# Kernel tuning notes

Hardware: AMD Instinct MI355X
Metric: run time of the kernel (lower is better)

## Reference

```python
import jax, jax.numpy as jnp
import numpy as np

N = 50000      # nodes
E = 800000     # directed edges (before self-loops)
FEAT = 120     # raw node feature dim
TOPO = 8       # topological feature dim
H1, D1 = 8, 8  # conv1: heads, per-head dim
C = 40         # out_channels (classes)
NEG_SLOPE = 0.2


def setup_inputs() -> dict:
    key = jax.random.key(0)
    ks = jax.random.split(key, 10)
    return {
        "x": jax.random.normal(ks[0], (N, FEAT), dtype=jnp.float32),
        "topo": jax.random.normal(ks[1], (N, TOPO), dtype=jnp.float32),
        "edge_index": jax.random.randint(ks[2], (2, E), 0, N, dtype=jnp.int32),
        "W1": jax.random.normal(ks[3], (FEAT + TOPO, H1 * D1), dtype=jnp.float32) * 0.1,
        "a_src1": jax.random.normal(ks[4], (H1, D1), dtype=jnp.float32) * 0.1,
        "a_dst1": jax.random.normal(ks[5], (H1, D1), dtype=jnp.float32) * 0.1,
        "b1": jnp.zeros((H1 * D1,), dtype=jnp.float32),
        "W2": jax.random.normal(ks[6], (H1 * D1, C), dtype=jnp.float32) * 0.1,
        "a_src2": jax.random.normal(ks[7], (1, C), dtype=jnp.float32) * 0.1,
        "a_dst2": jax.random.normal(ks[8], (1, C), dtype=jnp.float32) * 0.1,
        "b2": jnp.zeros((C,), dtype=jnp.float32),
    }


def gat_conv(x, src, dst, W, a_src, a_dst, b, heads, d, concat):
    """PyG-style GATConv (eval mode). src/dst already include self-loops."""
    n = x.shape[0]
    h = (x @ W).reshape(n, heads, d)                      # [N,H,D]
    al_src = jnp.sum(h * a_src[None], axis=-1)            # [N,H]
    al_dst = jnp.sum(h * a_dst[None], axis=-1)            # [N,H]
    e = jax.nn.leaky_relu(al_src[src] + al_dst[dst], NEG_SLOPE)  # [E',H]
    # segment softmax over incoming edges per destination node
    m = jax.ops.segment_max(e, dst, num_segments=n)       # [N,H]
    p = jnp.exp(e - m[dst])                               # [E',H]
    s = jax.ops.segment_sum(p, dst, num_segments=n)       # [N,H]
    alpha = p / s[dst]                                    # [E',H]
    out = jax.ops.segment_sum(alpha[:, :, None] * h[src], dst, num_segments=n)  # [N,H,D]
    if concat:
        return out.reshape(n, heads * d) + b
    return out.mean(axis=1) + b


def reference(x, topo, edge_index, W1, a_src1, a_dst1, b1, W2, a_src2, a_dst2, b2):
    n = x.shape[0]
    loops = jnp.arange(n, dtype=edge_index.dtype)
    src = jnp.concatenate([edge_index[0], loops])
    dst = jnp.concatenate([edge_index[1], loops])
    xin = jnp.concatenate([x, topo], axis=1)              # [N, FEAT+TOPO]
    h = jax.nn.elu(gat_conv(xin, src, dst, W1, a_src1, a_dst1, b1, H1, D1, True))
    out = gat_conv(h, src, dst, W2, a_src2, a_dst2, b2, 1, C, False)
    return jax.nn.log_softmax(out, axis=1)
```

## Files before the change

### kernel.cpp

```cpp
#include <hip/hip_runtime.h>
#include <hip/hip_fp16.h>

#define NN 50000
#define EE 800000
#define NBUCK 196
#define CAP 5120
#define TILEA 1024
#define NBA ((EE + TILEA - 1) / TILEA)
#define NGB 782
#define SRCS_MAX (EE + 8 * NN)

typedef _Float16 half8 __attribute__((ext_vector_type(8)));
typedef float floatx4 __attribute__((ext_vector_type(4)));

__global__ void k_prep(const float* __restrict__ W1, const float* __restrict__ W2,
                       _Float16* __restrict__ Bf1, _Float16* __restrict__ Bf2,
                       int* __restrict__ cursor, float* __restrict__ alsrc,
                       float* __restrict__ al2s) {
    int tid = blockIdx.x * 256 + threadIdx.x;
    if (tid < 1024) {
        int kk = tid >> 8, ct = (tid >> 6) & 3, L = tid & 63;
        int k0 = kk * 32 + (L >> 4) * 8, col = ct * 16 + (L & 15);
        half8 v;
        #pragma unroll
        for (int j = 0; j < 8; j++) v[j] = (_Float16)W1[(k0 + j) * 64 + col];
        *(half8*)(Bf1 + ((size_t)((kk * 4 + ct) * 64 + L)) * 8) = v;
    } else if (tid < 1024 + 384) {
        int u = tid - 1024;
        int kk = u / 192, rem = u % 192;
        int ct = rem >> 6, L = rem & 63;
        int k0 = kk * 32 + (L >> 4) * 8, col = ct * 16 + (L & 15);
        half8 v;
        #pragma unroll
        for (int j = 0; j < 8; j++)
            v[j] = (col < 40) ? (_Float16)W2[(k0 + j) * 40 + col] : (_Float16)0.f;
        *(half8*)(Bf2 + ((size_t)((kk * 3 + ct) * 64 + L)) * 8) = v;
    } else {
        int u = tid - 1408;
        if (u < NBUCK) cursor[u] = 0;
        if (u >= 200 && u < 208) alsrc[(size_t)NN * 8 + (u - 200)] = -1e30f;
        if (u == 208) al2s[NN] = -1e30f;
    }
}

__global__ __launch_bounds__(256) void k_fusedAG(
    const int* __restrict__ ei, int* __restrict__ cursor,
    unsigned* __restrict__ bucketData,
    const float* __restrict__ x, const float* __restrict__ topo,
    const _Float16* __restrict__ Bf1,
    const float* __restrict__ a_src, const float* __restrict__ a_dst,
    __half* __restrict__ h1, float* __restrict__ alsrc, float* __restrict__ aldst) {
    if (blockIdx.x < NBA) {
        __shared__ int cnt[NBUCK], base[NBUCK];
        int t = threadIdx.x;
        for (int i = t; i < NBUCK; i += 256) cnt[i] = 0;
        __syncthreads();
        int e0 = blockIdx.x * TILEA;
        int nE = min(TILEA, EE - e0);
        unsigned pk[4]; int bk[4], rk[4];
        int m = 0;
        for (int i = t; i < nE; i += 256) {
            int e = e0 + i;
            int s = ei[e], d = ei[EE + e];
            pk[m] = ((unsigned)d << 16) | (unsigned)s;
            bk[m] = d >> 8;
            rk[m] = atomicAdd(&cnt[bk[m]], 1);
            m++;
        }
        __syncthreads();
        for (int i = t; i < NBUCK; i += 256)
            base[i] = (cnt[i] > 0) ? atomicAdd(&cursor[i], cnt[i]) : 0;
        __syncthreads();
        for (int k = 0; k < m; k++) {
            int pos = base[bk[k]] + rk[k];
            if (pos < CAP) bucketData[(size_t)bk[k] * CAP + pos] = pk[k];
        }
        return;
    }
    int wave = threadIdx.x >> 6, lane = threadIdx.x & 63;
    int row0 = (blockIdx.x - NBA) * 64 + wave * 16;
    if (row0 >= NN) return;
    int g = lane >> 4, li = lane & 15;
    int myrow = row0 + li;
    half8 B[16];
    const half8* bp = (const half8*)Bf1;
    #pragma unroll
    for (int i = 0; i < 16; i++) B[i] = bp[i * 64 + lane];
    floatx4 acc[4] = {{0,0,0,0},{0,0,0,0},{0,0,0,0},{0,0,0,0}};
    #pragma unroll
    for (int kk = 0; kk < 4; kk++) {
        int k0 = kk * 32 + g * 8;
        const float* sp = (k0 == 120) ? (topo + (size_t)myrow * 8)
                                      : (x + (size_t)myrow * 120 + k0);
        float4 u0 = ((const float4*)sp)[0];
        float4 u1 = ((const float4*)sp)[1];
        half8 av;
        av[0] = (_Float16)u0.x; av[1] = (_Float16)u0.y;
        av[2] = (_Float16)u0.z; av[3] = (_Float16)u0.w;
        av[4] = (_Float16)u1.x; av[5] = (_Float16)u1.y;
        av[6] = (_Float16)u1.z; av[7] = (_Float16)u1.w;
        #pragma unroll
        for (int ct = 0; ct < 4; ct++)
            acc[ct] = __builtin_amdgcn_mfma_f32_16x16x32_f16(av, B[kk * 4 + ct], acc[ct], 0, 0, 0);
    }
    #pragma unroll
    for (int ct = 0; ct < 4; ct++)
        #pragma unroll
        for (int r = 0; r < 4; r++)
            h1[(size_t)(row0 + 4 * g + r) * 64 + ct * 16 + li] = __float2half(acc[ct][r]);
    float ps[4][4], pd[4][4];
    #pragma unroll
    for (int ct = 0; ct < 4; ct++) {
        int head = 2 * ct + (li >> 3), dix = li & 7;
        float asv = a_src[head * 8 + dix];
        float adv = a_dst[head * 8 + dix];
        #pragma unroll
        for (int r = 0; r < 4; r++) {
            ps[ct][r] = acc[ct][r] * asv;
            pd[ct][r] = acc[ct][r] * adv;
        }
    }
    #pragma unroll
    for (int off = 1; off <= 4; off <<= 1)
        #pragma unroll
        for (int ct = 0; ct < 4; ct++)
            #pragma unroll
            for (int r = 0; r < 4; r++) {
                ps[ct][r] += __shfl_xor(ps[ct][r], off, 64);
                pd[ct][r] += __shfl_xor(pd[ct][r], off, 64);
            }
    if ((li & 7) == 0) {
        #pragma unroll
        for (int ct = 0; ct < 4; ct++) {
            int head = 2 * ct + (li >> 3);
            #pragma unroll
            for (int r = 0; r < 4; r++) {
                int row = row0 + 4 * g + r;
                alsrc[row * 8 + head] = ps[ct][r];
                aldst[row * 8 + head] = pd[ct][r];
            }
        }
    }
}

__global__ __launch_bounds__(1024) void k_bucketB(const unsigned* __restrict__ bucketData,
        const int* __restrict__ cursor,
        int2* __restrict__ rowseg, int* __restrict__ srcs) {
    __shared__ int cnt[256], cur[256], sbuf[256], svals[256];
    __shared__ int sorted[CAP + 2048];
    int b = blockIdx.x, t = threadIdx.x;
    int nloc = min(256, NN - b * 256);
    int ecnt = min(cursor[b], CAP);
    size_t inBase = (size_t)b * CAP;
    if (t < 256) {
        int vv = 0;
        if (t < NBUCK) {
            int nl = min(256, NN - t * 256);
            vv = min(cursor[t], CAP) + 8 * nl;
        }
        svals[t] = vv;
    }
    __syncthreads();
    int* a = svals; int* bb = sbuf;
    for (int off = 1; off < 256; off <<= 1) {
        if (t < 256) bb[t] = a[t] + ((t >= off) ? a[t - off] : 0);
        __syncthreads();
        int* tmp = a; a = bb; bb = tmp;
    }
    int outBase = (b == 0) ? 0 : a[b - 1];
    __syncthreads();
    if (t < 256) cnt[t] = (t < nloc) ? 1 : 0;
    __syncthreads();
    for (int i = t; i < ecnt; i += 1024) {
        unsigned u = bucketData[inBase + i];
        atomicAdd(&cnt[(u >> 16) & 255], 1);
    }
    __syncthreads();
    int cv = 0, pcv = 0;
    if (t < 256) {
        cv = cnt[t];
        pcv = (t < nloc) ? ((cv + 7) & ~7) : 0;
        sbuf[t] = pcv;
    }
    __syncthreads();
    a = sbuf; bb = cnt;
    for (int off = 1; off < 256; off <<= 1) {
        if (t < 256) bb[t] = a[t] + ((t >= off) ? a[t - off] : 0);
        __syncthreads();
        int* tmp = a; a = bb; bb = tmp;
    }
    int total = a[255];
    int excl = (t < 256) ? (a[t] - pcv) : 0;
    __syncthreads();
    if (t < nloc) {
        rowseg[b * 256 + t] = make_int2(outBase + excl, outBase + excl + pcv);
        sorted[excl] = b * 256 + t;
        for (int k = cv; k < pcv; k++) sorted[excl + k] = NN;
        cur[t] = excl + 1;
    }
    __syncthreads();
    for (int i = t; i < ecnt; i += 1024) {
        unsigned u = bucketData[inBase + i];
        int ld = (u >> 16) & 255;
        int p = atomicAdd(&cur[ld], 1);
        sorted[p] = (int)(u & 0xffffu);
    }
    __syncthreads();
    for (int i = t; i < total; i += 1024) srcs[outBase + i] = sorted[i];
}

__global__ __launch_bounds__(256) void k_agg1(
    const int2* __restrict__ rowseg, const int* __restrict__ srcs,
    const float* __restrict__ alsrc, const float* __restrict__ aldst,
    const __half* __restrict__ h1, const float* __restrict__ b1,
    __half* __restrict__ hout) {
    int wave = threadIdx.x >> 6;
    int lane = threadIdx.x & 63;
    int d = blockIdx.x * 4 + wave;
    if (d >= NN) return;
    int hs = lane >> 5;
    int cp = lane & 31;
    int hh = cp >> 2;
    float adst = aldst[d * 8 + hh];
    int2 seg = rowseg[d];
    int jb = seg.x, je = seg.y;
    float ssum = 0.f, ax = 0.f, ay = 0.f;
    int sA0 = srcs[jb + hs],     sA1 = srcs[jb + 2 + hs];
    int sA2 = srcs[jb + 4 + hs], sA3 = srcs[jb + 6 + hs];
    for (int j = jb; j < je; j += 8) {
        int s0 = sA0, s1 = sA1, s2 = sA2, s3 = sA3;
        int jn = j + 8;
        if (jn < je) {
            sA0 = srcs[jn + hs];     sA1 = srcs[jn + 2 + hs];
            sA2 = srcs[jn + 4 + hs]; sA3 = srcs[jn + 6 + hs];
        }
        float e0 = alsrc[s0 * 8 + hh] + adst;
        float e1 = alsrc[s1 * 8 + hh] + adst;
        float e2 = alsrc[s2 * 8 + hh] + adst;
        float e3 = alsrc[s3 * 8 + hh] + adst;
        __half2 v0 = *(const __half2*)(h1 + (size_t)s0 * 64 + 2 * cp);
        __half2 v1 = *(const __half2*)(h1 + (size_t)s1 * 64 + 2 * cp);
        __half2 v2 = *(const __half2*)(h1 + (size_t)s2 * 64 + 2 * cp);
        __half2 v3 = *(const __half2*)(h1 + (size_t)s3 * 64 + 2 * cp);
        float p0 = __expf(fmaxf(e0, 0.2f * e0));
        float p1 = __expf(fmaxf(e1, 0.2f * e1));
        float p2 = __expf(fmaxf(e2, 0.2f * e2));
        float p3 = __expf(fmaxf(e3, 0.2f * e3));
        float2 f0 = __half22float2(v0), f1 = __half22float2(v1);
        float2 f2 = __half22float2(v2), f3 = __half22float2(v3);
        ssum += (p0 + p1) + (p2 + p3);
        ax += p0 * f0.x + p1 * f1.x + p2 * f2.x + p3 * f3.x;
        ay += p0 * f0.y + p1 * f1.y + p2 * f2.y + p3 * f3.y;
    }
    ssum += __shfl_xor(ssum, 32, 64);
    ax += __shfl_xor(ax, 32, 64);
    ay += __shfl_xor(ay, 32, 64);
    if (hs == 0) {
        float2 bv = *(const float2*)(b1 + 2 * cp);
        float inv = 1.f / ssum;
        float vx = ax * inv + bv.x;
        float vy = ay * inv + bv.y;
        vx = (vx > 0.f) ? vx : (__expf(vx) - 1.f);
        vy = (vy > 0.f) ? vy : (__expf(vy) - 1.f);
        *(__half2*)(hout + (size_t)d * 64 + 2 * cp) = __floats2half2_rn(vx, vy);
    }
}

__global__ __launch_bounds__(256) void k_gemm2(
    const __half* __restrict__ hout, const _Float16* __restrict__ Bf2,
    const float* __restrict__ a_src2, const float* __restrict__ a_dst2,
    __half* __restrict__ h2, float* __restrict__ al2s, float* __restrict__ al2d) {
    int wave = threadIdx.x >> 6, lane = threadIdx.x & 63;
    int row0 = blockIdx.x * 64 + wave * 16;
    if (row0 >= NN) return;
    int g = lane >> 4, li = lane & 15;
    int myrow = row0 + li;
    half8 B[6];
    const half8* bp = (const half8*)Bf2;
    #pragma unroll
    for (int i = 0; i < 6; i++) B[i] = bp[i * 64 + lane];
    floatx4 acc[3] = {{0,0,0,0},{0,0,0,0},{0,0,0,0}};
    #pragma unroll
    for (int kk = 0; kk < 2; kk++) {
        int k0 = kk * 32 + g * 8;
        half8 av = *(const half8*)(hout + (size_t)myrow * 64 + k0);
        #pragma unroll
        for (int ct = 0; ct < 3; ct++)
            acc[ct] = __builtin_amdgcn_mfma_f32_16x16x32_f16(av, B[kk * 3 + ct], acc[ct], 0, 0, 0);
    }
    float ts[4] = {0.f, 0.f, 0.f, 0.f}, td[4] = {0.f, 0.f, 0.f, 0.f};
    #pragma unroll
    for (int ct = 0; ct < 3; ct++) {
        int col = ct * 16 + li;
        bool ok = (col < 40);
        float asv = ok ? a_src2[col] : 0.f;
        float adv = ok ? a_dst2[col] : 0.f;
        #pragma unroll
        for (int r = 0; r < 4; r++) {
            ts[r] += acc[ct][r] * asv;
            td[r] += acc[ct][r] * adv;
            if (ok) h2[(size_t)(row0 + 4 * g + r) * 40 + col] = __float2half(acc[ct][r]);
        }
    }
    #pragma unroll
    for (int off = 1; off <= 8; off <<= 1)
        #pragma unroll
        for (int r = 0; r < 4; r++) {
            ts[r] += __shfl_xor(ts[r], off, 64);
            td[r] += __shfl_xor(td[r], off, 64);
        }
    if (li == 0) {
        #pragma unroll
        for (int r = 0; r < 4; r++) {
            int row = row0 + 4 * g + r;
            al2s[row] = ts[r];
            al2d[row] = td[r];
        }
    }
}

__global__ __launch_bounds__(256) void k_agg2(
    const int2* __restrict__ rowseg, const int* __restrict__ srcs,
    const float* __restrict__ al2s, const float* __restrict__ al2d,
    const __half* __restrict__ h2, const float* __restrict__ b2,
    float* __restrict__ out) {
    int wave = threadIdx.x >> 6;
    int lane = threadIdx.x & 63;
    int d = blockIdx.x * 4 + wave;
    if (d >= NN) return;
    int hs = lane >> 5;
    int cp = lane & 31;
    bool act = (cp < 20);
    int cpc = act ? cp : 0;
    float adst = al2d[d];
    int2 seg = rowseg[d];
    int jb = seg.x, je = seg.y;
    float ssum = 0.f, ax = 0.f, ay = 0.f;
    int sA0 = srcs[jb + hs],     sA1 = srcs[jb + 2 + hs];
    int sA2 = srcs[jb + 4 + hs], sA3 = srcs[jb + 6 + hs];
    for (int j = jb; j < je; j += 8) {
        int s0 = sA0, s1 = sA1, s2 = sA2, s3 = sA3;
        int jn = j + 8;
        if (jn < je) {
            sA0 = srcs[jn + hs];     sA1 = srcs[jn + 2 + hs];
            sA2 = srcs[jn + 4 + hs]; sA3 = srcs[jn + 6 + hs];
        }
        float e0 = al2s[s0] + adst;
        float e1 = al2s[s1] + adst;
        float e2 = al2s[s2] + adst;
        float e3 = al2s[s3] + adst;
        __half2 v0 = *(const __half2*)(h2 + (size_t)s0 * 40 + 2 * cpc);
        __half2 v1 = *(const __half2*)(h2 + (size_t)s1 * 40 + 2 * cpc);
        __half2 v2 = *(const __half2*)(h2 + (size_t)s2 * 40 + 2 * cpc);
        __half2 v3 = *(const __half2*)(h2 + (size_t)s3 * 40 + 2 * cpc);
        float p0 = __expf(fmaxf(e0, 0.2f * e0));
        float p1 = __expf(fmaxf(e1, 0.2f * e1));
        float p2 = __expf(fmaxf(e2, 0.2f * e2));
        float p3 = __expf(fmaxf(e3, 0.2f * e3));
        float2 f0 = __half22float2(v0), f1 = __half22float2(v1);
        float2 f2 = __half22float2(v2), f3 = __half22float2(v3);
        ssum += (p0 + p1) + (p2 + p3);
        ax += p0 * f0.x + p1 * f1.x + p2 * f2.x + p3 * f3.x;
        ay += p0 * f0.y + p1 * f1.y + p2 * f2.y + p3 * f3.y;
    }
    ssum += __shfl_xor(ssum, 32, 64);
    ax += __shfl_xor(ax, 32, 64);
    ay += __shfl_xor(ay, 32, 64);
    float inv = 1.f / ssum;
    float2 bv = *(const float2*)(b2 + 2 * cpc);
    float ox = ax * inv + bv.x;
    float oy = ay * inv + bv.y;
    float mo = act ? fmaxf(ox, oy) : -3.0e38f;
    #pragma unroll
    for (int off = 16; off; off >>= 1) mo = fmaxf(mo, __shfl_xor(mo, off, 64));
    float te = act ? (__expf(ox - mo) + __expf(oy - mo)) : 0.f;
    #pragma unroll
    for (int off = 16; off; off >>= 1) te += __shfl_xor(te, off, 64);
    float ls = __logf(te);
    if (act && hs == 0)
        *(float2*)(out + (size_t)d * 40 + 2 * cp) = make_float2(ox - mo - ls, oy - mo - ls);
}

extern "C" void kernel_launch(void* const* d_in, const int* in_sizes, int n_in,
                              void* d_out, int out_size, void* d_ws, size_t ws_size,
                              hipStream_t stream) {
    (void)in_sizes; (void)n_in; (void)out_size; (void)ws_size;
    const float* x    = (const float*)d_in[0];
    const float* topo = (const float*)d_in[1];
    const int*   ei   = (const int*)d_in[2];
    const float* W1   = (const float*)d_in[3];
    const float* as1  = (const float*)d_in[4];
    const float* ad1  = (const float*)d_in[5];
    const float* b1   = (const float*)d_in[6];
    const float* W2   = (const float*)d_in[7];
    const float* as2  = (const float*)d_in[8];
    const float* ad2  = (const float*)d_in[9];
    const float* b2   = (const float*)d_in[10];
    float* out = (float*)d_out;

    char* ws = (char*)d_ws;
    size_t off = 0;
    auto alloc = [&](size_t bytes) {
        void* p = ws + off;
        off += (bytes + 255) / 256 * 256;
        return p;
    };
    int2*      rowseg     = (int2*)alloc((size_t)NN * 8);
    int*       cursor     = (int*)alloc(NBUCK * 4);
    unsigned*  bucketData = (unsigned*)alloc((size_t)NBUCK * CAP * 4);
    int*       srcs       = (int*)alloc((size_t)SRCS_MAX * 4);
    float*     alsrc1     = (float*)alloc((size_t)(NN + 1) * 8 * 4);
    float*     aldst1     = (float*)alloc((size_t)NN * 8 * 4);
    float*     al2s       = (float*)alloc((NN + 1) * 4);
    float*     al2d       = (float*)alloc(NN * 4);
    _Float16*  Bf1        = (_Float16*)alloc(4 * 4 * 64 * 8 * 2);
    _Float16*  Bf2        = (_Float16*)alloc(2 * 3 * 64 * 8 * 2);
    __half*    h1         = (__half*)alloc((size_t)(NN + 1) * 64 * 2);
    __half*    hout       = (__half*)alloc((size_t)NN * 64 * 2);
    __half*    h2         = (__half*)alloc((size_t)(NN + 1) * 40 * 2);

    k_prep    <<<7,         256,  0, stream>>>(W1, W2, Bf1, Bf2, cursor, alsrc1, al2s);
    k_fusedAG <<<NBA + NGB, 256,  0, stream>>>(ei, cursor, bucketData,
                                               x, topo, Bf1, as1, ad1, h1, alsrc1, aldst1);
    k_bucketB <<<NBUCK,     1024, 0, stream>>>(bucketData, cursor, rowseg, srcs);
    k_agg1    <<<(NN + 3) / 4, 256, 0, stream>>>(rowseg, srcs, alsrc1, aldst1, h1, b1, hout);
    k_gemm2   <<<NGB,       256,  0, stream>>>(hout, Bf2, as2, ad2, h2, al2s, al2d);
    k_agg2    <<<(NN + 3) / 4, 256, 0, stream>>>(rowseg, srcs, al2s, al2d, h2, b2, out);
}
```

Before: 182.8 us.

## Regroup kernels: fold weight prep into bucket pass A, GEMM1 into bucket pass B

The weight-conversion prep kernel becomes extra blocks of the edge-bucketing kernel, and the layer-1 MFMA GEMM with its attention logits becomes extra 1024-thread blocks of the per-bucket sort kernel, so the GEMM overlaps the sort rather than the first bucketing pass. The cursor reset moves to hipMemsetAsync. The B fragments are now loaded per k-step to reduce register pressure under the 1024-thread launch bound. The trade-off is that the GEMM blocks now carry the sort kernel's large static shared-memory footprint and 1024-thread shape, which may lower occupancy.

```diff
diff --git a/kernel.cpp b/kernel.cpp
--- a/kernel.cpp
+++ b/kernel.cpp
@@ -7,49 +7,16 @@
 #define CAP 5120
 #define TILEA 1024
 #define NBA ((EE + TILEA - 1) / TILEA)
-#define NGB 782
 #define SRCS_MAX (EE + 8 * NN)
 
 typedef _Float16 half8 __attribute__((ext_vector_type(8)));
 typedef float floatx4 __attribute__((ext_vector_type(4)));
 
-__global__ void k_prep(const float* __restrict__ W1, const float* __restrict__ W2,
-                       _Float16* __restrict__ Bf1, _Float16* __restrict__ Bf2,
-                       int* __restrict__ cursor, float* __restrict__ alsrc,
-                       float* __restrict__ al2s) {
-    int tid = blockIdx.x * 256 + threadIdx.x;
-    if (tid < 1024) {
-        int kk = tid >> 8, ct = (tid >> 6) & 3, L = tid & 63;
-        int k0 = kk * 32 + (L >> 4) * 8, col = ct * 16 + (L & 15);
-        half8 v;
-        #pragma unroll
-        for (int j = 0; j < 8; j++) v[j] = (_Float16)W1[(k0 + j) * 64 + col];
-        *(half8*)(Bf1 + ((size_t)((kk * 4 + ct) * 64 + L)) * 8) = v;
-    } else if (tid < 1024 + 384) {
-        int u = tid - 1024;
-        int kk = u / 192, rem = u % 192;
-        int ct = rem >> 6, L = rem & 63;
-        int k0 = kk * 32 + (L >> 4) * 8, col = ct * 16 + (L & 15);
-        half8 v;
-        #pragma unroll
-        for (int j = 0; j < 8; j++)
-            v[j] = (col < 40) ? (_Float16)W2[(k0 + j) * 40 + col] : (_Float16)0.f;
-        *(half8*)(Bf2 + ((size_t)((kk * 3 + ct) * 64 + L)) * 8) = v;
-    } else {
-        int u = tid - 1408;
-        if (u < NBUCK) cursor[u] = 0;
-        if (u >= 200 && u < 208) alsrc[(size_t)NN * 8 + (u - 200)] = -1e30f;
-        if (u == 208) al2s[NN] = -1e30f;
-    }
-}
-
-__global__ __launch_bounds__(256) void k_fusedAG(
-    const int* __restrict__ ei, int* __restrict__ cursor,
-    unsigned* __restrict__ bucketData,
-    const float* __restrict__ x, const float* __restrict__ topo,
-    const _Float16* __restrict__ Bf1,
-    const float* __restrict__ a_src, const float* __restrict__ a_dst,
-    __half* __restrict__ h1, float* __restrict__ alsrc, float* __restrict__ aldst) {
+__global__ __launch_bounds__(256) void k_A(const int* __restrict__ ei,
+        int* __restrict__ cursor, unsigned* __restrict__ bucketData,
+        const float* __restrict__ W1, const float* __restrict__ W2,
+        _Float16* __restrict__ Bf1, _Float16* __restrict__ Bf2,
+        float* __restrict__ alsrc, float* __restrict__ al2s) {
     if (blockIdx.x < NBA) {
         __shared__ int cnt[NBUCK], base[NBUCK];
         int t = threadIdx.x;
@@ -77,18 +44,114 @@
         }
         return;
     }
+    int tid = (blockIdx.x - NBA) * 256 + threadIdx.x;
+    if (tid < 1024) {
+        int kk = tid >> 8, ct = (tid >> 6) & 3, L = tid & 63;
+        int k0 = kk * 32 + (L >> 4) * 8, col = ct * 16 + (L & 15);
+        half8 v;
+        #pragma unroll
+        for (int j = 0; j < 8; j++) v[j] = (_Float16)W1[(k0 + j) * 64 + col];
+        *(half8*)(Bf1 + ((size_t)((kk * 4 + ct) * 64 + L)) * 8) = v;
+    } else if (tid < 1024 + 384) {
+        int u = tid - 1024;
+        int kk = u / 192, rem = u % 192;
+        int ct = rem >> 6, L = rem & 63;
+        int k0 = kk * 32 + (L >> 4) * 8, col = ct * 16 + (L & 15);
+        half8 v;
+        #pragma unroll
+        for (int j = 0; j < 8; j++)
+            v[j] = (col < 40) ? (_Float16)W2[(k0 + j) * 40 + col] : (_Float16)0.f;
+        *(half8*)(Bf2 + ((size_t)((kk * 3 + ct) * 64 + L)) * 8) = v;
+    } else {
+        int u = tid - 1408;
+        if (u < 8) alsrc[(size_t)NN * 8 + u] = -1e30f;
+        if (u == 8) al2s[NN] = -1e30f;
+    }
+}
+
+__global__ __launch_bounds__(1024) void k_B(const unsigned* __restrict__ bucketData,
+        const int* __restrict__ cursor,
+        int2* __restrict__ rowseg, int* __restrict__ srcs,
+        const float* __restrict__ x, const float* __restrict__ topo,
+        const _Float16* __restrict__ Bf1,
+        const float* __restrict__ a_src, const float* __restrict__ a_dst,
+        __half* __restrict__ h1, float* __restrict__ alsrc, float* __restrict__ aldst) {
+    __shared__ int cnt[256], cur[256], sbuf[256], svals[256];
+    __shared__ int sorted[CAP + 2048];
+    if (blockIdx.x < NBUCK) {
+        int b = blockIdx.x, t = threadIdx.x;
+        int nloc = min(256, NN - b * 256);
+        int ecnt = min(cursor[b], CAP);
+        size_t inBase = (size_t)b * CAP;
+        if (t < 256) {
+            int vv = 0;
+            if (t < NBUCK) {
+                int nl = min(256, NN - t * 256);
+                vv = min(cursor[t], CAP) + 8 * nl;
+            }
+            svals[t] = vv;
+        }
+        __syncthreads();
+        int* a = svals; int* bb = sbuf;
+        for (int off = 1; off < 256; off <<= 1) {
+            if (t < 256) bb[t] = a[t] + ((t >= off) ? a[t - off] : 0);
+            __syncthreads();
+            int* tmp = a; a = bb; bb = tmp;
+        }
+        int outBase = (b == 0) ? 0 : a[b - 1];
+        __syncthreads();
+        if (t < 256) cnt[t] = (t < nloc) ? 1 : 0;
+        __syncthreads();
+        for (int i = t; i < ecnt; i += 1024) {
+            unsigned u = bucketData[inBase + i];
+            atomicAdd(&cnt[(u >> 16) & 255], 1);
+        }
+        __syncthreads();
+        int cv = 0, pcv = 0;
+        if (t < 256) {
+            cv = cnt[t];
+            pcv = (t < nloc) ? ((cv + 7) & ~7) : 0;
+            sbuf[t] = pcv;
+        }
+        __syncthreads();
+        a = sbuf; bb = cnt;
+        for (int off = 1; off < 256; off <<= 1) {
+            if (t < 256) bb[t] = a[t] + ((t >= off) ? a[t - off] : 0);
+            __syncthreads();
+            int* tmp = a; a = bb; bb = tmp;
+        }
+        int total = a[255];
+        int excl = (t < 256) ? (a[t] - pcv) : 0;
+        __syncthreads();
+        if (t < nloc) {
+            rowseg[b * 256 + t] = make_int2(outBase + excl, outBase + excl + pcv);
+            sorted[excl] = b * 256 + t;
+            for (int k = cv; k < pcv; k++) sorted[excl + k] = NN;
+            cur[t] = excl + 1;
+        }
+        __syncthreads();
+        for (int i = t; i < ecnt; i += 1024) {
+            unsigned u = bucketData[inBase + i];
+            int ld = (u >> 16) & 255;
+            int p = atomicAdd(&cur[ld], 1);
+            sorted[p] = (int)(u & 0xffffu);
+        }
+        __syncthreads();
+        for (int i = t; i < total; i += 1024) srcs[outBase + i] = sorted[i];
+        return;
+    }
     int wave = threadIdx.x >> 6, lane = threadIdx.x & 63;
-    int row0 = (blockIdx.x - NBA) * 64 + wave * 16;
+    int row0 = (blockIdx.x - NBUCK) * 256 + wave * 16;
     if (row0 >= NN) return;
     int g = lane >> 4, li = lane & 15;
     int myrow = row0 + li;
-    half8 B[16];
     const half8* bp = (const half8*)Bf1;
-    #pragma unroll
-    for (int i = 0; i < 16; i++) B[i] = bp[i * 64 + lane];
     floatx4 acc[4] = {{0,0,0,0},{0,0,0,0},{0,0,0,0},{0,0,0,0}};
     #pragma unroll
     for (int kk = 0; kk < 4; kk++) {
+        half8 Bv[4];
+        #pragma unroll
+        for (int ct = 0; ct < 4; ct++) Bv[ct] = bp[(kk * 4 + ct) * 64 + lane];
         int k0 = kk * 32 + g * 8;
         const float* sp = (k0 == 120) ? (topo + (size_t)myrow * 8)
                                       : (x + (size_t)myrow * 120 + k0);
@@ -101,7 +164,7 @@
         av[6] = (_Float16)u1.z; av[7] = (_Float16)u1.w;
         #pragma unroll
         for (int ct = 0; ct < 4; ct++)
-            acc[ct] = __builtin_amdgcn_mfma_f32_16x16x32_f16(av, B[kk * 4 + ct], acc[ct], 0, 0, 0);
+            acc[ct] = __builtin_amdgcn_mfma_f32_16x16x32_f16(av, Bv[ct], acc[ct], 0, 0, 0);
     }
     #pragma unroll
     for (int ct = 0; ct < 4; ct++)
@@ -141,72 +204,6 @@
             }
         }
     }
-}
-
-__global__ __launch_bounds__(1024) void k_bucketB(const unsigned* __restrict__ bucketData,
-        const int* __restrict__ cursor,
-        int2* __restrict__ rowseg, int* __restrict__ srcs) {
-    __shared__ int cnt[256], cur[256], sbuf[256], svals[256];
-    __shared__ int sorted[CAP + 2048];
-    int b = blockIdx.x, t = threadIdx.x;
-    int nloc = min(256, NN - b * 256);
-    int ecnt = min(cursor[b], CAP);
-    size_t inBase = (size_t)b * CAP;
-    if (t < 256) {
-        int vv = 0;
-        if (t < NBUCK) {
-            int nl = min(256, NN - t * 256);
-            vv = min(cursor[t], CAP) + 8 * nl;
-        }
-        svals[t] = vv;
-    }
-    __syncthreads();
-    int* a = svals; int* bb = sbuf;
-    for (int off = 1; off < 256; off <<= 1) {
-        if (t < 256) bb[t] = a[t] + ((t >= off) ? a[t - off] : 0);
-        __syncthreads();
-        int* tmp = a; a = bb; bb = tmp;
-    }
-    int outBase = (b == 0) ? 0 : a[b - 1];
-    __syncthreads();
-    if (t < 256) cnt[t] = (t < nloc) ? 1 : 0;
-    __syncthreads();
-    for (int i = t; i < ecnt; i += 1024) {
-        unsigned u = bucketData[inBase + i];
-        atomicAdd(&cnt[(u >> 16) & 255], 1);
-    }
-    __syncthreads();
-    int cv = 0, pcv = 0;
-    if (t < 256) {
-        cv = cnt[t];
-        pcv = (t < nloc) ? ((cv + 7) & ~7) : 0;
-        sbuf[t] = pcv;
-    }
-    __syncthreads();
-    a = sbuf; bb = cnt;
-    for (int off = 1; off < 256; off <<= 1) {
-        if (t < 256) bb[t] = a[t] + ((t >= off) ? a[t - off] : 0);
-        __syncthreads();
-        int* tmp = a; a = bb; bb = tmp;
-    }
-    int total = a[255];
-    int excl = (t < 256) ? (a[t] - pcv) : 0;
-    __syncthreads();
-    if (t < nloc) {
-        rowseg[b * 256 + t] = make_int2(outBase + excl, outBase + excl + pcv);
-        sorted[excl] = b * 256 + t;
-        for (int k = cv; k < pcv; k++) sorted[excl + k] = NN;
-        cur[t] = excl + 1;
-    }
-    __syncthreads();
-    for (int i = t; i < ecnt; i += 1024) {
-        unsigned u = bucketData[inBase + i];
-        int ld = (u >> 16) & 255;
-        int p = atomicAdd(&cur[ld], 1);
-        sorted[p] = (int)(u & 0xffffu);
-    }
-    __syncthreads();
-    for (int i = t; i < total; i += 1024) srcs[outBase + i] = sorted[i];
 }
 
 __global__ __launch_bounds__(256) void k_agg1(
@@ -419,11 +416,12 @@
     __half*    hout       = (__half*)alloc((size_t)NN * 64 * 2);
     __half*    h2         = (__half*)alloc((size_t)(NN + 1) * 40 * 2);
 
-    k_prep    <<<7,         256,  0, stream>>>(W1, W2, Bf1, Bf2, cursor, alsrc1, al2s);
-    k_fusedAG <<<NBA + NGB, 256,  0, stream>>>(ei, cursor, bucketData,
+    hipMemsetAsync(cursor, 0, NBUCK * 4, stream);
+    k_A     <<<NBA + 6,    256,  0, stream>>>(ei, cursor, bucketData, W1, W2,
+                                              Bf1, Bf2, alsrc1, al2s);
+    k_B     <<<NBUCK + 196, 1024, 0, stream>>>(bucketData, cursor, rowseg, srcs,
                                                x, topo, Bf1, as1, ad1, h1, alsrc1, aldst1);
-    k_bucketB <<<NBUCK,     1024, 0, stream>>>(bucketData, cursor, rowseg, srcs);
-    k_agg1    <<<(NN + 3) / 4, 256, 0, stream>>>(rowseg, srcs, alsrc1, aldst1, h1, b1, hout);
-    k_gemm2   <<<NGB,       256,  0, stream>>>(hout, Bf2, as2, ad2, h2, al2s, al2d);
-    k_agg2    <<<(NN + 3) / 4, 256, 0, stream>>>(rowseg, srcs, al2s, al2d, h2, b2, out);
-}
+    k_agg1  <<<(NN + 3) / 4, 256, 0, stream>>>(rowseg, srcs, alsrc1, aldst1, h1, b1, hout);
+    k_gemm2 <<<782,        256,  0, stream>>>(hout, Bf2, as2, ad2, h2, al2s, al2d);
+    k_agg2  <<<(NN + 3) / 4, 256, 0, stream>>>(rowseg, srcs, al2s, al2d, h2, b2, out);
+}
```

Measured after the change: 184.0 us. About the same (+0.6%).
